# Kernel optimization log

Hardware: AMD Instinct MI355X
Metric: run time of the kernel (lower is better)

## Reference

```python
import jax, jax.numpy as jnp
import numpy as np


def _gru_cell(x, h, Wih, Whh, bih, bhh):
    # PyTorch GRU cell (seq_len=1): gates ordered r, z, n
    gi = x @ Wih.T + bih
    gh = h @ Whh.T + bhh
    i_r, i_z, i_n = jnp.split(gi, 3, axis=-1)
    h_r, h_z, h_n = jnp.split(gh, 3, axis=-1)
    r = jax.nn.sigmoid(i_r + h_r)
    z = jax.nn.sigmoid(i_z + h_z)
    n = jnp.tanh(i_n + r * h_n)
    return (1.0 - z) * n + z * h


def setup_inputs() -> dict:
    key = jax.random.key(0)
    N, K, n_in, H = 4096, 8, 14, 128
    ks = jax.random.split(key, 24)
    s = 0.05
    inp = {
        "towers": jax.random.normal(ks[0], (N, K, n_in), jnp.float32),
        # E_n encoder (Linear -> tanh -> Linear -> tanh)
        "En_W1": jax.random.normal(ks[1], (H, n_in)) * s,
        "En_b1": jnp.zeros((H,)),
        "En_W2": jax.random.normal(ks[2], (H, H)) * s,
        "En_b2": jnp.zeros((H,)),
        # E_e encoder
        "Ee_W1": jax.random.normal(ks[3], (H, 2 * n_in)) * s,
        "Ee_b1": jnp.zeros((H,)),
        "Ee_W2": jax.random.normal(ks[4], (H, H)) * s,
        "Ee_b2": jnp.zeros((H,)),
        # U_gru (node update), input n_in + H
        "U_Wih": jax.random.normal(ks[5], (3 * H, n_in + H)) * s,
        "U_Whh": jax.random.normal(ks[6], (3 * H, H)) * s,
        "U_bih": jnp.zeros((3 * H,)),
        "U_bhh": jnp.zeros((3 * H,)),
        # M_gru (edge update), input 2*(n_in + H)
        "M_Wih": jax.random.normal(ks[7], (3 * H, 2 * (n_in + H))) * s,
        "M_Whh": jax.random.normal(ks[8], (3 * H, H)) * s,
        "M_bih": jnp.zeros((3 * H,)),
        "M_bhh": jnp.zeros((3 * H,)),
        # G_gru (global update), input 2*H
        "G_Wih": jax.random.normal(ks[9], (3 * H, 2 * H)) * s,
        "G_Whh": jax.random.normal(ks[10], (3 * H, H)) * s,
        "G_bih": jnp.zeros((3 * H,)),
        "G_bhh": jnp.zeros((3 * H,)),
        # output head
        "O_W": jax.random.normal(ks[11], (1, H)) * s,
        "O_b": jnp.zeros((1,)),
        "k": 3,
    }
    return inp


def reference(towers, En_W1, En_b1, En_W2, En_b2, Ee_W1, Ee_b1, Ee_W2, Ee_b2,
              U_Wih, U_Whh, U_bih, U_bhh, M_Wih, M_Whh, M_bih, M_bhh,
              G_Wih, G_Whh, G_bih, G_bhh, O_W, O_b, k):
    N, K, n_in = towers.shape
    H = En_W1.shape[0]
    # node state init: h = E_n(towers)
    h = jnp.tanh(jnp.tanh(towers @ En_W1.T + En_b1) @ En_W2.T + En_b2)  # (N,K,H)
    # edge state init: e_h = E_e(all-pairs concat of towers)
    xi = jnp.broadcast_to(towers[:, :, None, :], (N, K, K, n_in))
    xj = jnp.broadcast_to(towers[:, None, :, :], (N, K, K, n_in))
    xx0 = jnp.concatenate([xi, xj], axis=-1)  # (N,K,K,2*n_in)
    e_h = jnp.tanh(jnp.tanh(xx0 @ Ee_W1.T + Ee_b1) @ Ee_W2.T + Ee_b2)  # (N,K,K,H)
    # mask[i,j] = 1 iff j == i+1 (the nested-loop mask is a shifted identity)
    mask = jnp.eye(K, k=1, dtype=towers.dtype)
    e = e_h
    D = n_in + H
    for _ in range(k):
        # edge_fn: all-pairs concat of [towers, h] fed through GRU cell
        xh = jnp.concatenate([towers, h], axis=-1)  # (N,K,D)
        a = jnp.broadcast_to(xh[:, :, None, :], (N, K, K, D))
        b = jnp.broadcast_to(xh[:, None, :, :], (N, K, K, D))
        exx = jnp.concatenate([a, b], axis=-1).reshape(-1, 2 * D)
        e_h = _gru_cell(exx, e_h.reshape(-1, H), M_Wih, M_Whh, M_bih, M_bhh)
        e = e_h.reshape(N, K, K, H)
        # node_fn: masked sum selects e[:, i, i+1]
        edges = jnp.einsum('nijh,ij->nih', e, mask)  # (N,K,H)
        nx = jnp.concatenate([towers, edges], axis=-1).reshape(-1, D)
        h = _gru_cell(nx, h.reshape(-1, H), U_Wih, U_Whh, U_bih, U_bhh).reshape(N, K, H)
        e_h = e_h  # state carried
    # global_fn
    h_sum = h.sum(axis=1)  # (N,H)
    e_sum = jnp.einsum('nijh,ij->nh', e, mask)  # (N,H)
    gx = jnp.concatenate([h_sum, e_sum], axis=-1)  # (N,2H)
    g = _gru_cell(gx, jnp.zeros((N, H), towers.dtype), G_Wih, G_Whh, G_bih, G_bhh)
    out = jax.nn.sigmoid((g @ O_W.T + O_b).reshape(N))
    return out
```

## Files before the change

### kernel.cpp

```cpp
#include <hip/hip_runtime.h>
#include <hip/hip_bf16.h>

typedef __hip_bfloat16 bf16;
typedef unsigned short ush;
typedef short s16x8 __attribute__((ext_vector_type(8)));
typedef ush u16x4 __attribute__((ext_vector_type(4)));
typedef float f32x4 __attribute__((ext_vector_type(4)));

#define DEV __device__ __forceinline__

DEV float rcp_f(float x) { return __builtin_amdgcn_rcpf(x); }
DEV float sigmoid_f(float x) { return rcp_f(1.f + __expf(-x)); }
DEV float tanh_f(float x) { return 1.f - 2.f * rcp_f(__expf(2.f * x) + 1.f); }

DEV float u2f(ush u) { unsigned int v = ((unsigned int)u) << 16; float f; __builtin_memcpy(&f, &v, 4); return f; }
DEV ush f2u(float f) { bf16 h = __float2bfloat16(f); ush u; __builtin_memcpy(&u, &h, 2); return u; }

DEV f32x4 MFMA(s16x8 a, s16x8 b, f32x4 c) {
  return __builtin_amdgcn_mfma_f32_16x16x32_bf16(a, b, c, 0, 0, 0);
}

DEV s16x8 z8() {
  s16x8 v;
  for (int z = 0; z < 8; ++z) v[z] = 0;
  return v;
}

DEV int swz_idx(int row, int kk) { return row * 32 + (((kk >> 3) ^ ((row >> 1) & 3)) << 3) + (kk & 7); }
DEV int swz_blk(int row, int blk) { return row * 32 + ((blk ^ ((row >> 1) & 3)) << 3); }


__global__ __launch_bounds__(256) void prep_all(
    const float* __restrict__ towers,
    const float* __restrict__ MWih, const float* __restrict__ MWhh,
    const float* __restrict__ UWih, const float* __restrict__ UWhh,
    const float* __restrict__ EnW1, const float* __restrict__ EnW2,
    const float* __restrict__ EeW1, const float* __restrict__ EeW2,
    const float* __restrict__ MBih, const float* __restrict__ MBhh,
    const float* __restrict__ UBih, const float* __restrict__ UBhh,
    const float* __restrict__ GWih, const float* __restrict__ GWhh,
    const float* __restrict__ GBih, const float* __restrict__ GBhh,
    ush* __restrict__ xh, ush* __restrict__ WIHe, ush* __restrict__ WTh,
    ush* __restrict__ WTu, ush* __restrict__ WBen1, ush* __restrict__ WBen2,
    ush* __restrict__ WBee1, ush* __restrict__ WBee2,
    float* __restrict__ biasM, float* __restrict__ biasU,
    float* __restrict__ WT_G, float* __restrict__ biasG)
{
  const int b = blockIdx.x, t = threadIdx.x;
  if (b < 2048) {
    const int idx = b * 256 + t;
    const int row = idx >> 4, kk = idx & 15;
    xh[row * 144 + kk] = f2u(kk < 14 ? towers[row * 14 + kk] : 0.f);
  } else if (b < 2480) {
    const int idx = (b - 2048) * 256 + t;
    const int ck = idx / 12288, rem = idx % 12288, n = rem >> 5, kk = rem & 31;
    const int k = ck * 32 + kk;
    const int gate = n >> 7, c = n & 127;
    const int row = gate * 128 + c;
    int col = -1;
    if (k < 14)                    col = k;
    else if (k >= 16 && k < 144)   col = 14 + (k - 16);
    else if (k >= 144 && k < 158)  col = 142 + (k - 144);
    else if (k >= 160)             col = 156 + (k - 160);
    WIHe[idx] = f2u((col >= 0) ? MWih[row * 284 + col] : 0.f);
  } else if (b < 2672) {
    const int idx = (b - 2480) * 256 + t;
    const int ck = idx / 12288, rem = idx % 12288, n = rem >> 5, kk = rem & 31;
    const int g = n >> 7, c = n & 127;
    WTh[idx] = f2u(MWhh[(g * 128 + c) * 128 + ck * 32 + kk]);
  } else if (b < 3248) {
    const int idx = (b - 2672) * 256 + t;
    const int ck = idx >> 14, n = (idx >> 5) & 511, kk = idx & 31;
    const int k = ck * 32 + kk, gate = n >> 7, c = n & 127;
    float w = 0.f;
    const int row = (gate == 0) ? c : (gate == 1) ? 128 + c : 256 + c;
    if (k < 160) {
      int col = -1;
      if (k < 16)        { if (k < 14) col = k; }
      else if (k < 144)  col = 14 + (k - 16);
      if (gate != 3 && col >= 0) w = UWih[row * 142 + col];
    } else {
      if (gate != 2) w = UWhh[row * 128 + (k - 160)];
    }
    WTu[ck * 16384 + swz_idx(n, kk)] = f2u(w);
  } else if (b < 3264) {
    const int idx = (b - 3248) * 256 + t;
    const int n = (idx >> 5) & 127, kk = idx & 31;
    WBen1[idx] = f2u(kk < 14 ? EnW1[n * 14 + kk] : 0.f);
  } else if (b < 3328) {
    const int idx = (b - 3264) * 256 + t;
    const int ck = idx >> 12, n = (idx >> 5) & 127, kk = idx & 31;
    WBen2[idx] = f2u(EnW2[n * 128 + ck * 32 + kk]);
  } else if (b < 3344) {
    const int idx = (b - 3328) * 256 + t;
    const int n = (idx >> 5) & 127, kk = idx & 31;
    int col = (kk < 16) ? (kk < 14 ? kk : -1) : (kk < 30 ? 14 + (kk - 16) : -1);
    WBee1[idx] = f2u(col >= 0 ? EeW1[n * 28 + col] : 0.f);
    (void)n;
  } else if (b < 3408) {
    const int idx = (b - 3344) * 256 + t;
    const int ck = idx >> 12, n = (idx >> 5) & 127, kk = idx & 31;
    WBee2[idx] = f2u(EeW2[n * 128 + ck * 32 + kk]);
  } else if (b < 3410) {
    const int idx = (b - 3408) * 256 + t;
    const int g = idx >> 7, c = idx & 127;
    float v;
    if (g == 0)      v = MBih[c] + MBhh[c];
    else if (g == 1) v = MBih[128 + c] + MBhh[128 + c];
    else if (g == 2) v = MBih[256 + c];
    else             v = MBhh[256 + c];
    biasM[idx] = v;
  } else if (b < 3412) {
    const int idx = (b - 3410) * 256 + t;
    const int g = idx >> 7, c = idx & 127;
    float v;
    if (g == 0)      v = UBih[c] + UBhh[c];
    else if (g == 1) v = UBih[128 + c] + UBhh[128 + c];
    else if (g == 2) v = UBih[256 + c];
    else             v = UBhh[256 + c];
    biasU[idx] = v;
  } else if (b < 4180) {
    const int idx = (b - 3412) * 256 + t;
    const int kc = idx >> 9, cg = (idx >> 2) & 127, gate = idx & 3;
    const int row = (gate == 0) ? cg : (gate == 1) ? cg + 128 : cg + 256;
    float v = 0.f;
    if (kc < 256) { if (gate != 3) v = GWih[row * 256 + kc]; }
    else          { if (gate != 2) v = GWhh[row * 128 + (kc - 256)]; }
    WT_G[idx] = v;
  } else {
    const int idx = (b - 4180) * 256 + t;
    const int cg = idx >> 2, gate = idx & 3;
    float v;
    if (gate == 0)      v = GBih[cg] + GBhh[cg];
    else if (gate == 1) v = GBih[cg + 128] + GBhh[cg + 128];
    else if (gate == 2) v = GBih[cg + 256];
    else                v = GBhh[cg + 256];
    biasG[idx] = v;
  }
}

__global__ __launch_bounds__(256, 2) void enc_en(
    ush* __restrict__ xh,
    const ush* __restrict__ WB1, const float* __restrict__ b1,
    const ush* __restrict__ WB2, const float* __restrict__ b2)
{
  __shared__ ush smem[9216];
  ush* A1 = smem;
  ush* Z1 = smem + 1024;
  const int t = threadIdx.x, lane = t & 63, w = t >> 6;
  const int rowBase = blockIdx.x * 64;
  const int quad = lane >> 4, l15 = lane & 15;

  {
    const int gm = t >> 2, gb = t & 3, grow = rowBase + gm;
    s16x8 v = z8();
    if (gb < 2) v = *(const s16x8*)(xh + grow * 144 + gb * 8);
    *(s16x8*)&A1[swz_blk(gm, gb)] = v;
  }
  __syncthreads();

  s16x8 af[4];
  #pragma unroll
  for (int rt = 0; rt < 4; ++rt)
    af[rt] = *(const s16x8*)&A1[swz_blk(rt * 16 + l15, quad)];
  f32x4 acc1[4][2];
  #pragma unroll
  for (int rt = 0; rt < 4; ++rt)
    #pragma unroll
    for (int ct = 0; ct < 2; ++ct) {
      #pragma unroll
      for (int q = 0; q < 4; ++q) acc1[rt][ct][q] = 0.f;
    }
  #pragma unroll
  for (int ct = 0; ct < 2; ++ct) {
    const int n = w * 32 + ct * 16 + l15;
    const s16x8 bf = *(const s16x8*)&WB1[n * 32 + quad * 8];
    #pragma unroll
    for (int rt = 0; rt < 4; ++rt) acc1[rt][ct] = MFMA(af[rt], bf, acc1[rt][ct]);
  }
  #pragma unroll
  for (int ct = 0; ct < 2; ++ct) {
    const int col = w * 32 + ct * 16 + l15;
    const int kk = col & 31;
    #pragma unroll
    for (int rt = 0; rt < 4; ++rt) {
      #pragma unroll
      for (int q = 0; q < 4; ++q) {
        const int m = rt * 16 + quad * 4 + q;
        Z1[w * 2048 + swz_idx(m, kk)] = f2u(tanh_f(acc1[rt][ct][q] + b1[col]));
      }
    }
  }
  __syncthreads();

  f32x4 acc2[4][2];
  #pragma unroll
  for (int rt = 0; rt < 4; ++rt)
    #pragma unroll
    for (int ct = 0; ct < 2; ++ct) {
      #pragma unroll
      for (int q = 0; q < 4; ++q) acc2[rt][ct][q] = 0.f;
    }
  for (int ck2 = 0; ck2 < 4; ++ck2) {
    #pragma unroll
    for (int rt = 0; rt < 4; ++rt)
      af[rt] = *(const s16x8*)&Z1[ck2 * 2048 + swz_blk(rt * 16 + l15, quad)];
    #pragma unroll
    for (int ct = 0; ct < 2; ++ct) {
      const int n = w * 32 + ct * 16 + l15;
      const s16x8 bf = *(const s16x8*)&WB2[(ck2 * 128 + n) * 32 + quad * 8];
      #pragma unroll
      for (int rt = 0; rt < 4; ++rt) acc2[rt][ct] = MFMA(af[rt], bf, acc2[rt][ct]);
    }
  }

  #pragma unroll
  for (int ct = 0; ct < 2; ++ct) {
    const int col = w * 32 + ct * 16 + l15;
    #pragma unroll
    for (int rt = 0; rt < 4; ++rt) {
      #pragma unroll
      for (int q = 0; q < 4; ++q) {
        const int r = rt * 16 + quad * 4 + q;
        xh[(rowBase + r) * 144 + 16 + col] = f2u(tanh_f(acc2[rt][ct][q] + b2[col]));
      }
    }
  }
}

DEV void ee_body(ush* As_e, ush* SC, const ush* __restrict__ xh,
                 const ush* __restrict__ WB1, const float* __restrict__ b1,
                 const ush* __restrict__ WB2, const float* __restrict__ b2,
                 int G0, int t)
{
  ush* A1 = SC;
  ush* Z1 = SC + 1024;
  const int lane = t & 63, w = t >> 6;
  const int quad = lane >> 4, l15 = lane & 15;

  {
    const int gm = t >> 2, gb = t & 3;
    const int gg = gm >> 3, i = gm & 7;
    const int xi = (G0 + gg) * 8 + i;
    const int xj = (i < 7) ? xi + 1 : xi;
    const s16x8 v = (gb < 2) ? *(const s16x8*)(xh + xi * 144 + gb * 8)
                             : *(const s16x8*)(xh + xj * 144 + (gb - 2) * 8);
    *(s16x8*)&A1[swz_blk(gm, gb)] = v;
  }
  __syncthreads();

  s16x8 af[4];
  #pragma unroll
  for (int rt = 0; rt < 4; ++rt)
    af[rt] = *(const s16x8*)&A1[swz_blk(rt * 16 + l15, quad)];
  f32x4 acc1[4][2];
  #pragma unroll
  for (int rt = 0; rt < 4; ++rt)
    #pragma unroll
    for (int ct = 0; ct < 2; ++ct) {
      #pragma unroll
      for (int q = 0; q < 4; ++q) acc1[rt][ct][q] = 0.f;
    }
  #pragma unroll
  for (int ct = 0; ct < 2; ++ct) {
    const int n = w * 32 + ct * 16 + l15;
    const s16x8 bf = *(const s16x8*)&WB1[n * 32 + quad * 8];
    #pragma unroll
    for (int rt = 0; rt < 4; ++rt) acc1[rt][ct] = MFMA(af[rt], bf, acc1[rt][ct]);
  }
  #pragma unroll
  for (int ct = 0; ct < 2; ++ct) {
    const int col = w * 32 + ct * 16 + l15;
    const int kk = col & 31;
    #pragma unroll
    for (int rt = 0; rt < 4; ++rt) {
      #pragma unroll
      for (int q = 0; q < 4; ++q) {
        const int m = rt * 16 + quad * 4 + q;
        Z1[w * 2048 + swz_idx(m, kk)] = f2u(tanh_f(acc1[rt][ct][q] + b1[col]));
      }
    }
  }
  __syncthreads();

  f32x4 acc2[4][2];
  #pragma unroll
  for (int rt = 0; rt < 4; ++rt)
    #pragma unroll
    for (int ct = 0; ct < 2; ++ct) {
      #pragma unroll
      for (int q = 0; q < 4; ++q) acc2[rt][ct][q] = 0.f;
    }
  for (int ck2 = 0; ck2 < 4; ++ck2) {
    #pragma unroll
    for (int rt = 0; rt < 4; ++rt)
      af[rt] = *(const s16x8*)&Z1[ck2 * 2048 + swz_blk(rt * 16 + l15, quad)];
    #pragma unroll
    for (int ct = 0; ct < 2; ++ct) {
      const int n = w * 32 + ct * 16 + l15;
      const s16x8 bf = *(const s16x8*)&WB2[(ck2 * 128 + n) * 32 + quad * 8];
      #pragma unroll
      for (int rt = 0; rt < 4; ++rt) acc2[rt][ct] = MFMA(af[rt], bf, acc2[rt][ct]);
    }
  }
  #pragma unroll
  for (int ct = 0; ct < 2; ++ct) {
    const int col = w * 32 + ct * 16 + l15;
    const int kk = col & 31;
    #pragma unroll
    for (int rt = 0; rt < 4; ++rt) {
      #pragma unroll
      for (int q = 0; q < 4; ++q) {
        const int r = rt * 16 + quad * 4 + q;
        As_e[(col >> 5) * 2048 + swz_idx(r, kk)] = f2u(tanh_f(acc2[rt][ct][q] + b2[col]));
      }
    }
  }
}

template<int LAST>
DEV void edge_core(ush* As_e, ush* Bxx, ush* __restrict__ eh,
                   const ush* __restrict__ WIHe, const ush* __restrict__ WTh,
                   const float* __restrict__ biasM,
                   const ush* __restrict__ xh, int G0, int t)
{
  const int lane = t & 63, w = t >> 6;
  const int quad = lane >> 4, l15 = lane & 15;
  const int ko = quad * 8;

  f32x4 accR[2][4], accZ[2][4], accN1[2][4], accN2[2][4];
  #pragma unroll
  for (int mt = 0; mt < 2; ++mt)
    #pragma unroll
    for (int nt = 0; nt < 4; ++nt) {
      #pragma unroll
      for (int q = 0; q < 4; ++q) { accR[mt][nt][q] = 0.f; accZ[mt][nt][q] = 0.f; accN1[mt][nt][q] = 0.f; accN2[mt][nt][q] = 0.f; }
    }

  auto stage_xx = [&](int ck) {
    const int gm = t >> 2, gb = t & 3;
    const int gg = gm >> 3, i = gm & 7;
    const int xi = (G0 + gg) * 8 + i;
    const int xj = xi + ((i < 7) ? 1 : 0);
    const int k0 = ck * 32 + gb * 8;
    const s16x8 v = (k0 < 144) ? *(const s16x8*)(xh + xi * 144 + k0)
                               : *(const s16x8*)(xh + xj * 144 + (k0 - 144));
    *(s16x8*)&Bxx[(ck & 1) * 2048 + swz_blk(gm, gb)] = v;
  };

  stage_xx(0);
  __syncthreads();
  for (int ck = 0; ck < 9; ++ck) {
    if (ck + 1 < 9) stage_xx(ck + 1);
    const ush* Bc = Bxx + (ck & 1) * 2048;
    s16x8 be[4];
    #pragma unroll
    for (int nt = 0; nt < 4; ++nt)
      be[nt] = *(const s16x8*)&Bc[swz_blk(nt * 16 + l15, quad)];
    #pragma unroll
    for (int mt = 0; mt < 2; ++mt) {
      const int nb = w * 32 + mt * 16 + l15;
      const s16x8 aR = *(const s16x8*)&WIHe[(ck * 384 + nb) * 32 + ko];
      const s16x8 aZ = *(const s16x8*)&WIHe[(ck * 384 + 128 + nb) * 32 + ko];
      const s16x8 aN = *(const s16x8*)&WIHe[(ck * 384 + 256 + nb) * 32 + ko];
      #pragma unroll
      for (int nt = 0; nt < 4; ++nt) {
        accR[mt][nt]  = MFMA(aR, be[nt], accR[mt][nt]);
        accZ[mt][nt]  = MFMA(aZ, be[nt], accZ[mt][nt]);
        accN1[mt][nt] = MFMA(aN, be[nt], accN1[mt][nt]);
      }
    }
    __syncthreads();
  }

  #pragma unroll
  for (int ck = 0; ck < 4; ++ck) {
    s16x8 be[4];
    #pragma unroll
    for (int nt = 0; nt < 4; ++nt)
      be[nt] = *(const s16x8*)&As_e[ck * 2048 + swz_blk(nt * 16 + l15, quad)];
    #pragma unroll
    for (int mt = 0; mt < 2; ++mt) {
      const int nb = w * 32 + mt * 16 + l15;
      const s16x8 aR = *(const s16x8*)&WTh[(ck * 384 + nb) * 32 + ko];
      const s16x8 aZ = *(const s16x8*)&WTh[(ck * 384 + 128 + nb) * 32 + ko];
      const s16x8 aN = *(const s16x8*)&WTh[(ck * 384 + 256 + nb) * 32 + ko];
      #pragma unroll
      for (int nt = 0; nt < 4; ++nt) {
        accR[mt][nt]  = MFMA(aR, be[nt], accR[mt][nt]);
        accZ[mt][nt]  = MFMA(aZ, be[nt], accZ[mt][nt]);
        accN2[mt][nt] = MFMA(aN, be[nt], accN2[mt][nt]);
      }
    }
  }

  __syncthreads();

  #pragma unroll
  for (int mt = 0; mt < 2; ++mt) {
    const int hc0 = w * 32 + mt * 16 + quad * 4;
    const int ck2 = hc0 >> 5, kkB = hc0 & 31;
    #pragma unroll
    for (int nt = 0; nt < 4; ++nt) {
      const int erow = nt * 16 + l15;
      const int gg = erow >> 3, i = erow & 7;
      ush* cell = &As_e[ck2 * 2048 + swz_blk(erow, kkB >> 3) + (kkB & 7)];
      const u16x4 hp4 = *(const u16x4*)cell;
      u16x4 ov;
      #pragma unroll
      for (int q = 0; q < 4; ++q) {
        const int c = hc0 + q;
        const float rg = sigmoid_f(accR[mt][nt][q] + biasM[c]);
        const float zg = sigmoid_f(accZ[mt][nt][q] + biasM[128 + c]);
        const float nn = tanh_f(accN1[mt][nt][q] + biasM[256 + c]
                                + rg * (accN2[mt][nt][q] + biasM[384 + c]));
        const float hp = u2f(hp4[q]);
        ov[q] = f2u(nn + zg * (hp - nn));
      }
      *(u16x4*)cell = ov;
      if (!LAST && i < 7)
        *(u16x4*)&eh[(size_t)((G0 + gg) * 64 + i * 9 + 1) * 128 + hc0] = ov;
    }
  }
}

DEV void node_lds(const ush* As_e, ush* SC, ush* __restrict__ xh,
                  const ush* __restrict__ WT, const float* __restrict__ bias,
                  int rowBase, int t)
{
  constexpr int NCH = 9, XCH = 5;
  const int lane = t & 63, w = t >> 6;
  const int gm = t >> 2, gb = t & 3, grow = rowBase + gm;
  const int l15 = lane & 15, quad = lane >> 4;

  f32x4 accR[4][2], accZ[4][2], accN1[4][2], accN2[4][2];
  #pragma unroll
  for (int rt = 0; rt < 4; ++rt)
    #pragma unroll
    for (int s = 0; s < 2; ++s) {
      #pragma unroll
      for (int q = 0; q < 4; ++q) { accR[rt][s][q] = 0.f; accZ[rt][s][q] = 0.f; accN1[rt][s][q] = 0.f; accN2[rt][s][q] = 0.f; }
    }

  auto stage = [&](int ck) {
    const int k0 = ck * 32 + gb * 8;
    s16x8 v = z8();
    if (k0 < 16)       v = *(const s16x8*)(xh + grow * 144 + k0);
    else if (k0 < 144) {
      const int i = gm & 7;
      if (i < 7) {
        const int ke = k0 - 16;
        v = *(const s16x8*)&As_e[(ke >> 5) * 2048 + swz_blk(gm, (ke & 31) >> 3)];
      }
    } else if (k0 >= 160) {
      v = *(const s16x8*)(xh + grow * 144 + 16 + (k0 - 160));
    }
    *(s16x8*)&SC[(ck & 1) * 2048 + swz_blk(gm, gb)] = v;
  };

  stage(0);
  __syncthreads();

  for (int ck = 0; ck < NCH; ++ck) {
    if (ck + 1 < NCH) stage(ck + 1);

    const ush* Wc = WT + ck * 16384;
    const ush* Ac = SC + (ck & 1) * 2048;
    s16x8 af[4];
    #pragma unroll
    for (int rt = 0; rt < 4; ++rt)
      af[rt] = *(const s16x8*)&Ac[swz_blk(rt * 16 + l15, quad)];
    if (ck < XCH) {
      #pragma unroll
      for (int s = 0; s < 2; ++s) {
        const int nb = w * 32 + s * 16 + l15;
        const s16x8 bR = *(const s16x8*)&Wc[swz_blk(0 * 128 + nb, quad)];
        const s16x8 bZ = *(const s16x8*)&Wc[swz_blk(1 * 128 + nb, quad)];
        const s16x8 bN = *(const s16x8*)&Wc[swz_blk(2 * 128 + nb, quad)];
        #pragma unroll
        for (int rt = 0; rt < 4; ++rt) {
          accR[rt][s]  = MFMA(af[rt], bR, accR[rt][s]);
          accZ[rt][s]  = MFMA(af[rt], bZ, accZ[rt][s]);
          accN1[rt][s] = MFMA(af[rt], bN, accN1[rt][s]);
        }
      }
    } else {
      #pragma unroll
      for (int s = 0; s < 2; ++s) {
        const int nb = w * 32 + s * 16 + l15;
        const s16x8 bR = *(const s16x8*)&Wc[swz_blk(0 * 128 + nb, quad)];
        const s16x8 bZ = *(const s16x8*)&Wc[swz_blk(1 * 128 + nb, quad)];
        const s16x8 bN = *(const s16x8*)&Wc[swz_blk(3 * 128 + nb, quad)];
        #pragma unroll
        for (int rt = 0; rt < 4; ++rt) {
          accR[rt][s]  = MFMA(af[rt], bR, accR[rt][s]);
          accZ[rt][s]  = MFMA(af[rt], bZ, accZ[rt][s]);
          accN2[rt][s] = MFMA(af[rt], bN, accN2[rt][s]);
        }
      }
    }
    __syncthreads();
  }

  #pragma unroll
  for (int s = 0; s < 2; ++s) {
    const int hcol = w * 32 + s * 16 + l15;
    const float bR = bias[hcol], bZ = bias[128 + hcol], bN1 = bias[256 + hcol], bN2 = bias[384 + hcol];
    #pragma unroll
    for (int rt = 0; rt < 4; ++rt) {
      #pragma unroll
      for (int q = 0; q < 4; ++q) {
        const int r = rt * 16 + quad * 4 + q;
        const int row = rowBase + r;
        const float hp = u2f(xh[row * 144 + 16 + hcol]);
        const float rg = sigmoid_f(accR[rt][s][q] + bR);
        const float zg = sigmoid_f(accZ[rt][s][q] + bZ);
        const float nn = tanh_f(accN1[rt][s][q] + bN1 + rg * (accN2[rt][s][q] + bN2));
        xh[row * 144 + 16 + hcol] = f2u(nn + zg * (hp - nn));
      }
    }
  }
}

DEV void sums_body(const ush* As_e, const ush* __restrict__ xh,
                   float* __restrict__ hsum, float* __restrict__ esum,
                   int G0, int rowBase, int t)
{
  #pragma unroll
  for (int ii = 0; ii < 4; ++ii) {
    const int p = t + ii * 256;
    const int gg = p >> 7, hh = p & 127;
    float es = 0.f;
    #pragma unroll
    for (int i = 0; i < 7; ++i) {
      const int slot = gg * 8 + i;
      es += u2f(As_e[(hh >> 5) * 2048 + swz_idx(slot, hh & 31)]);
    }
    float hs = 0.f;
    #pragma unroll
    for (int i = 0; i < 8; ++i)
      hs += u2f(xh[(rowBase + gg * 8 + i) * 144 + 16 + hh]);
    hsum[(G0 + gg) * 128 + hh] = hs;
    esum[(G0 + gg) * 128 + hh] = es;
  }
}

template<int FIRST, int LAST>
__global__ __launch_bounds__(256, 2) void gn_iter(
    ush* __restrict__ eh, ush* __restrict__ xh,
    const ush* __restrict__ WIHe, const ush* __restrict__ WTh,
    const float* __restrict__ biasM,
    const ush* __restrict__ WTu, const float* __restrict__ biasU,
    const ush* __restrict__ WBee1, const float* __restrict__ bEe1,
    const ush* __restrict__ WBee2, const float* __restrict__ bEe2,
    float* __restrict__ hsum, float* __restrict__ esum)
{
  __shared__ ush smem[17408];
  ush* As_e = smem;
  ush* SC   = smem + 8192;
  const int t = threadIdx.x;
  const int G0 = blockIdx.x * 8, rowBase = blockIdx.x * 64;

  if (FIRST) {
    ee_body(As_e, SC, xh, WBee1, bEe1, WBee2, bEe2, G0, t);
  } else {
    const int gm = t >> 2, gb = t & 3;
    const int gg = gm >> 3, i = gm & 7;
    const ush* src = eh + (size_t)((G0 + gg) * 64 + i * 9 + 1) * 128;
    #pragma unroll
    for (int ck = 0; ck < 4; ++ck) {
      s16x8 v = z8();
      if (i < 7) v = *(const s16x8*)(src + ck * 32 + gb * 8);
      *(s16x8*)&As_e[ck * 2048 + swz_blk(gm, gb)] = v;
    }
  }
  __syncthreads();

  edge_core<LAST>(As_e, SC, eh, WIHe, WTh, biasM, xh, G0, t);
  __syncthreads();

  node_lds(As_e, SC, xh, WTu, biasU, rowBase, t);

  if (LAST) {
    __syncthreads();
    sums_body(As_e, xh, hsum, esum, G0, rowBase, t);
  }
}

__global__ __launch_bounds__(256) void gru_global_out(
    const float* __restrict__ hsum, const float* __restrict__ esum,
    const float* __restrict__ WT, const float* __restrict__ bias,
    const float* __restrict__ OW, const float* __restrict__ Ob,
    float* __restrict__ out)
{
  constexpr int KT = 384;
  __shared__ float4 ATl4[KT * 4];
  __shared__ float4 Bl4[16 * 128];
  __shared__ float gmat[16 * 128];
  __shared__ float red[16 * 4];
  float* ATl = (float*)ATl4;
  const int t = threadIdx.x;
  const int rowBase = blockIdx.x * 16;
  for (int idx = t; idx < KT * 16; idx += 256) {
    const int kc = idx >> 4, r = idx & 15, grow = rowBase + r;
    float v = 0.f;
    if (kc < 128)      v = hsum[grow * 128 + kc];
    else if (kc < 256) v = esum[grow * 128 + (kc - 128)];
    ATl[idx] = v;
  }
  const int c = t & 127, rh = t >> 7;
  float accR[8], accZ[8], accN1[8];
  #pragma unroll
  for (int rr = 0; rr < 8; ++rr) { accR[rr] = 0.f; accZ[rr] = 0.f; accN1[rr] = 0.f; }
  const float4* WT4 = (const float4*)WT;
  for (int ck = 0; ck < 16; ++ck) {
    __syncthreads();
    #pragma unroll
    for (int ii = 0; ii < 8; ++ii) { const int idx = t + ii * 256; Bl4[idx] = WT4[ck * 2048 + idx]; }
    __syncthreads();
    const int kb = ck * 16;
    #pragma unroll
    for (int kcl = 0; kcl < 16; ++kcl) {
      const float4 wv = Bl4[kcl * 128 + c];
      const float4 a0 = ATl4[(kb + kcl) * 4 + rh * 2];
      const float4 a1 = ATl4[(kb + kcl) * 4 + rh * 2 + 1];
      const float av[8] = {a0.x, a0.y, a0.z, a0.w, a1.x, a1.y, a1.z, a1.w};
      #pragma unroll
      for (int rr = 0; rr < 8; ++rr) {
        accR[rr]  += wv.x * av[rr];
        accZ[rr]  += wv.y * av[rr];
        accN1[rr] += wv.z * av[rr];
      }
    }
  }
  const float4 bb = ((const float4*)bias)[c];
  const float ow = OW[c];
  #pragma unroll
  for (int rr = 0; rr < 8; ++rr) {
    const float rg = sigmoid_f(accR[rr] + bb.x);
    const float zg = sigmoid_f(accZ[rr] + bb.y);
    const float nn = tanh_f(accN1[rr] + bb.z + rg * bb.w);
    gmat[(rh * 8 + rr) * 128 + c] = (1.f - zg) * nn * ow;
  }
  __syncthreads();
  if (t < 64) {
    const int r = t >> 2, part = t & 3;
    float s = 0.f;
    #pragma unroll
    for (int cc = 0; cc < 32; ++cc) s += gmat[r * 128 + part * 32 + cc];
    red[r * 4 + part] = s;
  }
  __syncthreads();
  if (t < 16) {
    const float s = red[t * 4] + red[t * 4 + 1] + red[t * 4 + 2] + red[t * 4 + 3];
    out[rowBase + t] = sigmoid_f(s + Ob[0]);
  }
}

extern "C" void kernel_launch(void* const* d_in, const int* in_sizes, int n_in,
                              void* d_out, int out_size, void* d_ws, size_t ws_size,
                              hipStream_t stream)
{
  (void)in_sizes; (void)n_in; (void)out_size; (void)ws_size;
  const float* towers = (const float*)d_in[0];
  const float* EnW1 = (const float*)d_in[1];
  const float* EnB1 = (const float*)d_in[2];
  const float* EnW2 = (const float*)d_in[3];
  const float* EnB2 = (const float*)d_in[4];
  const float* EeW1 = (const float*)d_in[5];
  const float* EeB1 = (const float*)d_in[6];
  const float* EeW2 = (const float*)d_in[7];
  const float* EeB2 = (const float*)d_in[8];
  const float* UWih = (const float*)d_in[9];
  const float* UWhh = (const float*)d_in[10];
  const float* UBih = (const float*)d_in[11];
  const float* UBhh = (const float*)d_in[12];
  const float* MWih = (const float*)d_in[13];
  const float* MWhh = (const float*)d_in[14];
  const float* MBih = (const float*)d_in[15];
  const float* MBhh = (const float*)d_in[16];
  const float* GWih = (const float*)d_in[17];
  const float* GWhh = (const float*)d_in[18];
  const float* GBih = (const float*)d_in[19];
  const float* GBhh = (const float*)d_in[20];
  const float* OW   = (const float*)d_in[21];
  const float* Ob   = (const float*)d_in[22];

  char* ws = (char*)d_ws;
  size_t off = 0;
  auto take = [&](size_t b) { void* p = ws + off; off = (off + b + 255) & ~(size_t)255; return p; };
  ush*   xh     = (ush*)take((size_t)32768 * 144 * 2);
  ush*   eh     = (ush*)take((size_t)262144 * 128 * 2);
  float* hsum   = (float*)take((size_t)4096 * 128 * 4);
  float* esum   = (float*)take((size_t)4096 * 128 * 4);
  ush*   WIHe   = (ush*)take((size_t)9 * 384 * 32 * 2);
  ush*   WTh    = (ush*)take((size_t)4 * 384 * 32 * 2);
  ush*   WTu    = (ush*)take((size_t)9 * 512 * 32 * 2);
  ush*   WBen1  = (ush*)take((size_t)128 * 32 * 2);
  ush*   WBen2  = (ush*)take((size_t)4 * 128 * 32 * 2);
  ush*   WBee1  = (ush*)take((size_t)128 * 32 * 2);
  ush*   WBee2  = (ush*)take((size_t)4 * 128 * 32 * 2);
  float* biasM  = (float*)take(512 * 4);
  float* biasU  = (float*)take(512 * 4);
  float* WT_G   = (float*)take((size_t)384 * 512 * 4);
  float* biasG  = (float*)take(512 * 4);

  prep_all<<<4182, 256, 0, stream>>>(
      towers, MWih, MWhh, UWih, UWhh, EnW1, EnW2, EeW1, EeW2,
      MBih, MBhh, UBih, UBhh, GWih, GWhh, GBih, GBhh,
      xh, WIHe, WTh, WTu, WBen1, WBen2, WBee1, WBee2,
      biasM, biasU, WT_G, biasG);

  enc_en<<<512, 256, 0, stream>>>(xh, WBen1, EnB1, WBen2, EnB2);

  gn_iter<1, 0><<<512, 256, 0, stream>>>(eh, xh, WIHe, WTh, biasM, WTu, biasU,
                                         WBee1, EeB1, WBee2, EeB2, hsum, esum);
  gn_iter<0, 0><<<512, 256, 0, stream>>>(eh, xh, WIHe, WTh, biasM, WTu, biasU,
                                         WBee1, EeB1, WBee2, EeB2, hsum, esum);
  gn_iter<0, 1><<<512, 256, 0, stream>>>(eh, xh, WIHe, WTh, biasM, WTu, biasU,
                                         WBee1, EeB1, WBee2, EeB2, hsum, esum);

  gru_global_out<<<256, 256, 0, stream>>>(hsum, esum, WT_G, biasG, OW, Ob, (float*)d_out);
}
```

Baseline: 244.5 us.

## Fuse encoder and all three GN iterations into one persistent kernel

Merges the node encoder, edge encoder and the three edge/node update iterations into a single kernel. Each block keeps its edge state resident in shared memory across iterations instead of writing it to a global eh buffer and reading it back. This removes four kernel launches and the global round-trips of edge state. The per-block work becomes longer and serial, and the block-local dependence of xh (neighbor i+1 within the same 8-group) has to hold for correctness.

```diff
diff --git a/kernel.cpp b/kernel.cpp
--- a/kernel.cpp
+++ b/kernel.cpp
@@ -139,116 +139,16 @@
   }
 }
 
-__global__ __launch_bounds__(256, 2) void enc_en(
-    ush* __restrict__ xh,
-    const ush* __restrict__ WB1, const float* __restrict__ b1,
-    const ush* __restrict__ WB2, const float* __restrict__ b2)
-{
-  __shared__ ush smem[9216];
-  ush* A1 = smem;
-  ush* Z1 = smem + 1024;
-  const int t = threadIdx.x, lane = t & 63, w = t >> 6;
-  const int rowBase = blockIdx.x * 64;
-  const int quad = lane >> 4, l15 = lane & 15;
-
-  {
-    const int gm = t >> 2, gb = t & 3, grow = rowBase + gm;
-    s16x8 v = z8();
-    if (gb < 2) v = *(const s16x8*)(xh + grow * 144 + gb * 8);
-    *(s16x8*)&A1[swz_blk(gm, gb)] = v;
-  }
-  __syncthreads();
-
-  s16x8 af[4];
-  #pragma unroll
-  for (int rt = 0; rt < 4; ++rt)
-    af[rt] = *(const s16x8*)&A1[swz_blk(rt * 16 + l15, quad)];
-  f32x4 acc1[4][2];
-  #pragma unroll
-  for (int rt = 0; rt < 4; ++rt)
-    #pragma unroll
-    for (int ct = 0; ct < 2; ++ct) {
-      #pragma unroll
-      for (int q = 0; q < 4; ++q) acc1[rt][ct][q] = 0.f;
-    }
-  #pragma unroll
-  for (int ct = 0; ct < 2; ++ct) {
-    const int n = w * 32 + ct * 16 + l15;
-    const s16x8 bf = *(const s16x8*)&WB1[n * 32 + quad * 8];
-    #pragma unroll
-    for (int rt = 0; rt < 4; ++rt) acc1[rt][ct] = MFMA(af[rt], bf, acc1[rt][ct]);
-  }
-  #pragma unroll
-  for (int ct = 0; ct < 2; ++ct) {
-    const int col = w * 32 + ct * 16 + l15;
-    const int kk = col & 31;
-    #pragma unroll
-    for (int rt = 0; rt < 4; ++rt) {
-      #pragma unroll
-      for (int q = 0; q < 4; ++q) {
-        const int m = rt * 16 + quad * 4 + q;
-        Z1[w * 2048 + swz_idx(m, kk)] = f2u(tanh_f(acc1[rt][ct][q] + b1[col]));
-      }
-    }
-  }
-  __syncthreads();
-
-  f32x4 acc2[4][2];
-  #pragma unroll
-  for (int rt = 0; rt < 4; ++rt)
-    #pragma unroll
-    for (int ct = 0; ct < 2; ++ct) {
-      #pragma unroll
-      for (int q = 0; q < 4; ++q) acc2[rt][ct][q] = 0.f;
-    }
-  for (int ck2 = 0; ck2 < 4; ++ck2) {
-    #pragma unroll
-    for (int rt = 0; rt < 4; ++rt)
-      af[rt] = *(const s16x8*)&Z1[ck2 * 2048 + swz_blk(rt * 16 + l15, quad)];
-    #pragma unroll
-    for (int ct = 0; ct < 2; ++ct) {
-      const int n = w * 32 + ct * 16 + l15;
-      const s16x8 bf = *(const s16x8*)&WB2[(ck2 * 128 + n) * 32 + quad * 8];
-      #pragma unroll
-      for (int rt = 0; rt < 4; ++rt) acc2[rt][ct] = MFMA(af[rt], bf, acc2[rt][ct]);
-    }
-  }
-
-  #pragma unroll
-  for (int ct = 0; ct < 2; ++ct) {
-    const int col = w * 32 + ct * 16 + l15;
-    #pragma unroll
-    for (int rt = 0; rt < 4; ++rt) {
-      #pragma unroll
-      for (int q = 0; q < 4; ++q) {
-        const int r = rt * 16 + quad * 4 + q;
-        xh[(rowBase + r) * 144 + 16 + col] = f2u(tanh_f(acc2[rt][ct][q] + b2[col]));
-      }
-    }
-  }
-}
-
-DEV void ee_body(ush* As_e, ush* SC, const ush* __restrict__ xh,
-                 const ush* __restrict__ WB1, const float* __restrict__ b1,
-                 const ush* __restrict__ WB2, const float* __restrict__ b2,
-                 int G0, int t)
+template<class PUT>
+DEV void mlp2_body(ush* SC, const ush* __restrict__ WB1, const float* __restrict__ b1,
+                   const ush* __restrict__ WB2, const float* __restrict__ b2,
+                   int t, PUT&& put)
 {
   ush* A1 = SC;
   ush* Z1 = SC + 1024;
   const int lane = t & 63, w = t >> 6;
   const int quad = lane >> 4, l15 = lane & 15;
 
-  {
-    const int gm = t >> 2, gb = t & 3;
-    const int gg = gm >> 3, i = gm & 7;
-    const int xi = (G0 + gg) * 8 + i;
-    const int xj = (i < 7) ? xi + 1 : xi;
-    const s16x8 v = (gb < 2) ? *(const s16x8*)(xh + xi * 144 + gb * 8)
-                             : *(const s16x8*)(xh + xj * 144 + (gb - 2) * 8);
-    *(s16x8*)&A1[swz_blk(gm, gb)] = v;
-  }
-  __syncthreads();
-
   s16x8 af[4];
   #pragma unroll
   for (int rt = 0; rt < 4; ++rt)
@@ -306,20 +206,18 @@
   #pragma unroll
   for (int ct = 0; ct < 2; ++ct) {
     const int col = w * 32 + ct * 16 + l15;
-    const int kk = col & 31;
     #pragma unroll
     for (int rt = 0; rt < 4; ++rt) {
       #pragma unroll
       for (int q = 0; q < 4; ++q) {
         const int r = rt * 16 + quad * 4 + q;
-        As_e[(col >> 5) * 2048 + swz_idx(r, kk)] = f2u(tanh_f(acc2[rt][ct][q] + b2[col]));
-      }
-    }
-  }
-}
-
-template<int LAST>
-DEV void edge_core(ush* As_e, ush* Bxx, ush* __restrict__ eh,
+        put(r, col, tanh_f(acc2[rt][ct][q] + b2[col]));
+      }
+    }
+  }
+}
+
+DEV void edge_core(ush* As_e, ush* Bxx,
                    const ush* __restrict__ WIHe, const ush* __restrict__ WTh,
                    const float* __restrict__ biasM,
                    const ush* __restrict__ xh, int G0, int t)
@@ -403,7 +301,6 @@
     #pragma unroll
     for (int nt = 0; nt < 4; ++nt) {
       const int erow = nt * 16 + l15;
-      const int gg = erow >> 3, i = erow & 7;
       ush* cell = &As_e[ck2 * 2048 + swz_blk(erow, kkB >> 3) + (kkB & 7)];
       const u16x4 hp4 = *(const u16x4*)cell;
       u16x4 ov;
@@ -418,8 +315,6 @@
         ov[q] = f2u(nn + zg * (hp - nn));
       }
       *(u16x4*)cell = ov;
-      if (!LAST && i < 7)
-        *(u16x4*)&eh[(size_t)((G0 + gg) * 64 + i * 9 + 1) * 128 + hc0] = ov;
     }
   }
 }
@@ -545,14 +440,15 @@
   }
 }
 
-template<int FIRST, int LAST>
-__global__ __launch_bounds__(256, 2) void gn_iter(
-    ush* __restrict__ eh, ush* __restrict__ xh,
+__global__ __launch_bounds__(256, 2) void gn_all(
+    ush* __restrict__ xh,
+    const ush* __restrict__ WBen1, const float* __restrict__ bEn1,
+    const ush* __restrict__ WBen2, const float* __restrict__ bEn2,
+    const ush* __restrict__ WBee1, const float* __restrict__ bEe1,
+    const ush* __restrict__ WBee2, const float* __restrict__ bEe2,
     const ush* __restrict__ WIHe, const ush* __restrict__ WTh,
     const float* __restrict__ biasM,
     const ush* __restrict__ WTu, const float* __restrict__ biasU,
-    const ush* __restrict__ WBee1, const float* __restrict__ bEe1,
-    const ush* __restrict__ WBee2, const float* __restrict__ bEe2,
     float* __restrict__ hsum, float* __restrict__ esum)
 {
   __shared__ ush smem[17408];
@@ -561,30 +457,44 @@
   const int t = threadIdx.x;
   const int G0 = blockIdx.x * 8, rowBase = blockIdx.x * 64;
 
-  if (FIRST) {
-    ee_body(As_e, SC, xh, WBee1, bEe1, WBee2, bEe2, G0, t);
-  } else {
+  {
+    const int gm = t >> 2, gb = t & 3, grow = rowBase + gm;
+    s16x8 v = z8();
+    if (gb < 2) v = *(const s16x8*)(xh + grow * 144 + gb * 8);
+    *(s16x8*)&SC[swz_blk(gm, gb)] = v;
+  }
+  __syncthreads();
+  mlp2_body(SC, WBen1, bEn1, WBen2, bEn2, t,
+            [&](int r, int col, float v) {
+              xh[(rowBase + r) * 144 + 16 + col] = f2u(v);
+            });
+  __syncthreads();
+
+  {
     const int gm = t >> 2, gb = t & 3;
     const int gg = gm >> 3, i = gm & 7;
-    const ush* src = eh + (size_t)((G0 + gg) * 64 + i * 9 + 1) * 128;
-    #pragma unroll
-    for (int ck = 0; ck < 4; ++ck) {
-      s16x8 v = z8();
-      if (i < 7) v = *(const s16x8*)(src + ck * 32 + gb * 8);
-      *(s16x8*)&As_e[ck * 2048 + swz_blk(gm, gb)] = v;
-    }
-  }
-  __syncthreads();
-
-  edge_core<LAST>(As_e, SC, eh, WIHe, WTh, biasM, xh, G0, t);
-  __syncthreads();
-
-  node_lds(As_e, SC, xh, WTu, biasU, rowBase, t);
-
-  if (LAST) {
+    const int xi = (G0 + gg) * 8 + i;
+    const int xj = (i < 7) ? xi + 1 : xi;
+    const s16x8 v = (gb < 2) ? *(const s16x8*)(xh + xi * 144 + gb * 8)
+                             : *(const s16x8*)(xh + xj * 144 + (gb - 2) * 8);
+    *(s16x8*)&SC[swz_blk(gm, gb)] = v;
+  }
+  __syncthreads();
+  mlp2_body(SC, WBee1, bEe1, WBee2, bEe2, t,
+            [&](int r, int col, float v) {
+              As_e[(col >> 5) * 2048 + swz_idx(r, col & 31)] = f2u(v);
+            });
+  __syncthreads();
+
+  #pragma unroll 1
+  for (int it = 0; it < 3; ++it) {
+    edge_core(As_e, SC, WIHe, WTh, biasM, xh, G0, t);
     __syncthreads();
-    sums_body(As_e, xh, hsum, esum, G0, rowBase, t);
-  }
+    node_lds(As_e, SC, xh, WTu, biasU, rowBase, t);
+    __syncthreads();
+  }
+
+  sums_body(As_e, xh, hsum, esum, G0, rowBase, t);
 }
 
 __global__ __launch_bounds__(256) void gru_global_out(
@@ -690,7 +600,6 @@
   size_t off = 0;
   auto take = [&](size_t b) { void* p = ws + off; off = (off + b + 255) & ~(size_t)255; return p; };
   ush*   xh     = (ush*)take((size_t)32768 * 144 * 2);
-  ush*   eh     = (ush*)take((size_t)262144 * 128 * 2);
   float* hsum   = (float*)take((size_t)4096 * 128 * 4);
   float* esum   = (float*)take((size_t)4096 * 128 * 4);
   ush*   WIHe   = (ush*)take((size_t)9 * 384 * 32 * 2);
@@ -711,14 +620,9 @@
       xh, WIHe, WTh, WTu, WBen1, WBen2, WBee1, WBee2,
       biasM, biasU, WT_G, biasG);
 
-  enc_en<<<512, 256, 0, stream>>>(xh, WBen1, EnB1, WBen2, EnB2);
-
-  gn_iter<1, 0><<<512, 256, 0, stream>>>(eh, xh, WIHe, WTh, biasM, WTu, biasU,
-                                         WBee1, EeB1, WBee2, EeB2, hsum, esum);
-  gn_iter<0, 0><<<512, 256, 0, stream>>>(eh, xh, WIHe, WTh, biasM, WTu, biasU,
-                                         WBee1, EeB1, WBee2, EeB2, hsum, esum);
-  gn_iter<0, 1><<<512, 256, 0, stream>>>(eh, xh, WIHe, WTh, biasM, WTu, biasU,
-                                         WBee1, EeB1, WBee2, EeB2, hsum, esum);
+  gn_all<<<512, 256, 0, stream>>>(
+      xh, WBen1, EnB1, WBen2, EnB2, WBee1, EeB1, WBee2, EeB2,
+      WIHe, WTh, biasM, WTu, biasU, hsum, esum);
 
   gru_global_out<<<256, 256, 0, stream>>>(hsum, esum, WT_G, biasG, OW, Ob, (float*)d_out);
 }
```

Measured after the change: 469.0 us. +91.9%, slower.
